# Optimization experiments

Measured on AMD Instinct MI355X. Metric: run time of the kernel, lower is better.

The kernel has to match this reference:

```python
import jax, jax.numpy as jnp
import numpy as np

N, C, OUT, S, NS = 8192, 256, 256, 8, 16  # points, in_planes, out_planes, share_planes, nsample
MID = OUT  # mid_planes = out_planes // 1
H = OUT // S  # linear_w bottleneck width
EPS = 1e-5


def _bn(x, g, b, m, v):
    # inference-mode BatchNorm1d over last (channel) dim
    return (x - m) * jax.lax.rsqrt(v + EPS) * g + b


def _knn_idx(p, k):
    # squared euclidean distances, (N,N); indices of k nearest (self included)
    sq = jnp.sum(p * p, axis=1)
    d = sq[:, None] + sq[None, :] - 2.0 * (p @ p.T)
    return jax.lax.top_k(-jax.lax.stop_gradient(d), k)[1]  # (N, k) int32


def setup_inputs() -> dict:
    key = jax.random.key(0)
    ks = jax.random.split(key, 24)
    g = lambda i, shape, s=0.05: jax.random.normal(ks[i], shape, jnp.float32) * s
    u = lambda i, shape: jax.random.uniform(ks[i], shape, dtype=jnp.float32)
    return {
        'p': u(0, (N, 3)),
        'x': g(1, (N, C), 1.0),
        'w_q': g(2, (C, MID)), 'b_q': jnp.zeros((MID,), jnp.float32),
        'w_k': g(3, (C, MID)), 'b_k': jnp.zeros((MID,), jnp.float32),
        'w_v': g(4, (C, OUT)), 'b_v': jnp.zeros((OUT,), jnp.float32),
        'p_w1': g(5, (3, 3), 0.5), 'p_b1': jnp.zeros((3,), jnp.float32),
        'p_bn_g': u(6, (3,)) + 0.5, 'p_bn_b': g(7, (3,), 0.1),
        'p_bn_m': g(8, (3,), 0.1), 'p_bn_v': u(9, (3,)) + 0.5,
        'p_w2': g(10, (3, OUT), 0.5), 'p_b2': jnp.zeros((OUT,), jnp.float32),
        'w_bn1_g': u(11, (MID,)) + 0.5, 'w_bn1_b': g(12, (MID,), 0.1),
        'w_bn1_m': g(13, (MID,), 0.1), 'w_bn1_v': u(14, (MID,)) + 0.5,
        'w_l1_w': g(15, (MID, H)), 'w_l1_b': jnp.zeros((H,), jnp.float32),
        'w_bn2_g': u(16, (H,)) + 0.5, 'w_bn2_b': g(17, (H,), 0.1),
        'w_bn2_m': g(18, (H,), 0.1), 'w_bn2_v': u(19, (H,)) + 0.5,
        'w_l2_w': g(20, (H, H)), 'w_l2_b': jnp.zeros((H,), jnp.float32),
    }


def reference(p, x, w_q, b_q, w_k, b_k, w_v, b_v,
              p_w1, p_b1, p_bn_g, p_bn_b, p_bn_m, p_bn_v, p_w2, p_b2,
              w_bn1_g, w_bn1_b, w_bn1_m, w_bn1_v, w_l1_w, w_l1_b,
              w_bn2_g, w_bn2_b, w_bn2_m, w_bn2_v, w_l2_w, w_l2_b):
    # PointTransformerLayer forward (single point cloud, o = [N])
    xq = x @ w_q + b_q            # (N, MID)
    xk = x @ w_k + b_k            # (N, MID)
    xv = x @ w_v + b_v            # (N, OUT)

    idx = _knn_idx(p, NS)         # (N, NS) KNN neighbor indices
    pr_xyz = p[idx] - p[:, None, :]   # (N, NS, 3) relative coords (with_xyz=True)
    xk_g = xk[idx]                # (N, NS, MID) gathered keys
    xv_g = xv[idx]                # (N, NS, OUT) gathered values

    # linear_p: Linear(3,3) -> BN -> ReLU -> Linear(3, OUT)
    pr = jax.nn.relu(_bn(pr_xyz @ p_w1 + p_b1, p_bn_g, p_bn_b, p_bn_m, p_bn_v))
    pr = pr @ p_w2 + p_b2         # (N, NS, OUT)

    # einops reduce 'n ns (i j)->n ns j' with j=MID is identity since MID==OUT
    r_qk = xk_g - xq[:, None, :] + pr   # (N, NS, MID)

    # linear_w: BN -> ReLU -> Linear(MID,H) -> BN -> ReLU -> Linear(H,H)
    w = jax.nn.relu(_bn(r_qk, w_bn1_g, w_bn1_b, w_bn1_m, w_bn1_v)) @ w_l1_w + w_l1_b
    w = jax.nn.relu(_bn(w, w_bn2_g, w_bn2_b, w_bn2_m, w_bn2_v)) @ w_l2_w + w_l2_b
    w = jax.nn.softmax(w, axis=1)       # softmax over neighbors (dim=1)

    v = (xv_g + pr).reshape(N, NS, S, H)      # 'n ns (s i) -> n ns s i'
    out = jnp.einsum('ntsi,nti->nsi', v, w)   # weighted aggregation over neighbors
    return out.reshape(N, OUT)
```

## Files before the change

### kernel.cpp

```cpp
#include <hip/hip_runtime.h>
#include <hip/hip_bf16.h>
#include <math.h>

#define N_PTS 8192
#define C_IN  256
#define OUT_C 256
#define NSAMP 16
#define H_W   32
#define EPSBN 1e-5f
#define GDIM  8
#define NCELL (GDIM * GDIM * GDIM)
#define CAPC  768
#define CAP_H 64

typedef short bf16x8 __attribute__((ext_vector_type(8)));
typedef float f32x4  __attribute__((ext_vector_type(4)));

__device__ __forceinline__ float dist2(const float4 a, const float4 b) {
  float dot = a.x * b.x + a.y * b.y + a.z * b.z;
  return a.w + b.w - 2.0f * dot;
}

__device__ __forceinline__ unsigned long long make_key(float d, int j) {
  unsigned int di = __float_as_uint(d);
  unsigned int ord = ((int)di >= 0) ? (di ^ 0x80000000u) : ~di;
  return ((unsigned long long)ord << 32) | (unsigned int)j;
}

__device__ __forceinline__ void chain_insert(unsigned long long (&ak)[16], unsigned long long key) {
  if (key < ak[0]) {
    #pragma unroll
    for (int s = 0; s < 15; ++s) {
      unsigned long long mn = ak[s] < key ? ak[s] : key;
      unsigned long long nx = ak[s + 1];
      ak[s] = nx > mn ? nx : mn;
    }
    ak[15] = ak[15] < key ? ak[15] : key;
  }
}

__device__ __forceinline__ float b2f(short s) {
  return __uint_as_float(((unsigned int)(unsigned short)s) << 16);
}
__device__ __forceinline__ short f2b(float v) {
  __hip_bfloat16 h = __float2bfloat16(v);
  short s;
  __builtin_memcpy(&s, &h, 2);
  return s;
}

__global__ __launch_bounds__(256) void prep_kernel(
    const float* __restrict__ p,
    const float* __restrict__ wq, const float* __restrict__ wk, const float* __restrict__ wv,
    const float* __restrict__ bq, const float* __restrict__ bk, const float* __restrict__ bv,
    const float* __restrict__ l1w, const float* __restrict__ l2w,
    const float* __restrict__ bn1g, const float* __restrict__ bn1b,
    const float* __restrict__ bn1m, const float* __restrict__ bn1v,
    float4* __restrict__ p4, __hip_bfloat16* __restrict__ Bp, float* __restrict__ biasp,
    __hip_bfloat16* __restrict__ l1wp, __hip_bfloat16* __restrict__ l2wp,
    float* __restrict__ sc1, float* __restrict__ of1,
    int* __restrict__ cursor, int* __restrict__ pt_cell) {
  int tid = blockIdx.x * blockDim.x + threadIdx.x;
  if (tid < 48 * 32 * 16 * 8) {
    int kj = tid & 7, n = (tid >> 3) & 15, kb = (tid >> 7) & 31, nt = tid >> 12;
    int k = kb * 8 + kj, col = nt * 16 + n;
    float v;
    if (col < 256)      v = wq[k * 256 + col];
    else if (col < 512) v = wk[k * 256 + (col - 256)];
    else                v = wv[k * 256 + (col - 512)];
    Bp[tid] = __float2bfloat16(v);
  }
  if (tid < 768) {
    biasp[tid] = tid < 256 ? bq[tid] : (tid < 512 ? bk[tid - 256] : bv[tid - 512]);
  }
  if (tid < 8192) {
    int kj = tid & 7, n = (tid >> 3) & 15, kb = (tid >> 7) & 31, nt = (tid >> 12) & 1;
    int k = kb * 8 + kj, col = nt * 16 + n;
    l1wp[tid] = __float2bfloat16(l1w[k * 32 + col]);
  }
  if (tid < 1024) {
    int kj = tid & 7, n = (tid >> 3) & 15, kb = (tid >> 7) & 3, nt = (tid >> 9) & 1;
    int k = kb * 8 + kj, col = nt * 16 + n;
    l2wp[tid] = __float2bfloat16(l2w[k * 32 + col]);
  }
  if (tid < 256) {
    float s1 = bn1g[tid] * rsqrtf(bn1v[tid] + EPSBN);
    sc1[tid] = s1;
    of1[tid] = bn1b[tid] - bn1m[tid] * s1;
  }
  if (tid < NCELL) cursor[tid] = 0;
  if (tid < N_PTS) {
    float px = p[tid * 3 + 0], py = p[tid * 3 + 1], pz = p[tid * 3 + 2];
    float sq = px * px;
    sq += py * py;
    sq += pz * pz;
    p4[tid] = make_float4(px, py, pz, sq);
    int cx = min(GDIM - 1, max(0, (int)(px * GDIM)));
    int cy = min(GDIM - 1, max(0, (int)(py * GDIM)));
    int cz = min(GDIM - 1, max(0, (int)(pz * GDIM)));
    pt_cell[tid] = (cz * GDIM + cy) * GDIM + cx;
  }
}

__global__ __launch_bounds__(512) void scatter_scan(
    const float4* __restrict__ p4, const int* __restrict__ pt_cell,
    int* __restrict__ cell_start, int* __restrict__ cursor,
    float4* __restrict__ sp4, int* __restrict__ sidx, int* __restrict__ rank) {
  __shared__ int buf[NCELL];
  const int t = threadIdx.x;
  buf[t] = 0;
  __syncthreads();
  for (int i = t; i < N_PTS; i += 512) atomicAdd(&buf[pt_cell[i]], 1);
  __syncthreads();
  for (int off = 1; off < NCELL; off <<= 1) {
    int add = (t >= off) ? buf[t - off] : 0;
    __syncthreads();
    buf[t] += add;
    __syncthreads();
  }
  if (blockIdx.x == 0) {
    cell_start[t + 1] = buf[t];
    if (t == 0) cell_start[0] = 0;
  }
  const int pid = blockIdx.x * 512 + t;
  const int c = pt_cell[pid];
  const int start = (c == 0) ? 0 : buf[c - 1];
  const int pos = start + atomicAdd(&cursor[c], 1);
  sp4[pos] = p4[pid];
  sidx[pos] = pid;
  rank[pid] = pos;
}

__global__ __launch_bounds__(256) void gemm_qkv_mfma(
    const float* __restrict__ x, const int* __restrict__ sidx,
    const __hip_bfloat16* __restrict__ Bp,
    const float* __restrict__ biasp, __hip_bfloat16* __restrict__ xqkv) {
  const int w = threadIdx.x >> 6;
  const int lane = threadIdx.x & 63;
  const int gw = blockIdx.x * 4 + w;
  const int m0 = (gw & 127) * 64;
  const int nt4 = (gw >> 7) * 4;
  const int n = lane & 15, q = lane >> 4;

  int o[4];
  #pragma unroll
  for (int mi = 0; mi < 4; ++mi) o[mi] = sidx[m0 + mi * 16 + n];

  f32x4 acc[4][4];
  #pragma unroll
  for (int mi = 0; mi < 4; ++mi)
    #pragma unroll
    for (int ni = 0; ni < 4; ++ni) acc[mi][ni] = (f32x4){0.f, 0.f, 0.f, 0.f};

  for (int k0 = 0; k0 < 256; k0 += 32) {
    bf16x8 af[4], bfr[4];
    #pragma unroll
    for (int mi = 0; mi < 4; ++mi) {
      const float* xr = &x[(size_t)o[mi] * 256 + k0 + q * 8];
      float4 xa = *(const float4*)xr;
      float4 xb = *(const float4*)(xr + 4);
      af[mi][0] = f2b(xa.x); af[mi][1] = f2b(xa.y);
      af[mi][2] = f2b(xa.z); af[mi][3] = f2b(xa.w);
      af[mi][4] = f2b(xb.x); af[mi][5] = f2b(xb.y);
      af[mi][6] = f2b(xb.z); af[mi][7] = f2b(xb.w);
    }
    #pragma unroll
    for (int ni = 0; ni < 4; ++ni)
      bfr[ni] = *(const bf16x8*)&Bp[(size_t)(nt4 + ni) * 4096 + (k0 >> 3) * 128 + q * 128 + n * 8];
    #pragma unroll
    for (int mi = 0; mi < 4; ++mi)
      #pragma unroll
      for (int ni = 0; ni < 4; ++ni)
        acc[mi][ni] = __builtin_amdgcn_mfma_f32_16x16x32_bf16(af[mi], bfr[ni], acc[mi][ni], 0, 0, 0);
  }
  #pragma unroll
  for (int ni = 0; ni < 4; ++ni) {
    int col = (nt4 + ni) * 16 + n;
    float b = biasp[col];
    #pragma unroll
    for (int mi = 0; mi < 4; ++mi)
      #pragma unroll
      for (int r = 0; r < 4; ++r)
        xqkv[(size_t)(m0 + mi * 16 + q * 4 + r) * 768 + col] = __float2bfloat16(acc[mi][ni][r] + b);
  }
}

__global__ __launch_bounds__(256) void knn_grid(
    const float4* __restrict__ sp4, const int* __restrict__ sidx,
    const int* __restrict__ cell_start, int* __restrict__ nbr) {
  __shared__ float4 cpos[CAPC];
  __shared__ int    cidx[CAPC];
  __shared__ unsigned long long hk_s[8][CAP_H];
  __shared__ unsigned long long okey_s[8][16];
  __shared__ float tv_s[8][64];
  __shared__ int cnt_s[8];
  __shared__ int cell_s0_s[27];
  __shared__ int len_s[27];
  __shared__ int pref_s[28];
  __shared__ int nc_s, total_s;

  const int cell = blockIdx.x >> 1;
  const int sub  = blockIdx.x & 1;
  const int tid = threadIdx.x;
  const int hcx = cell & 7, hcy = (cell >> 3) & 7, hcz = cell >> 6;
  const int cs = cell_start[cell], ce = cell_start[cell + 1];

  const int ax0 = max(hcx - 1, 0), ax1 = min(hcx + 1, GDIM - 1);
  const int ay0 = max(hcy - 1, 0), ay1 = min(hcy + 1, GDIM - 1);
  const int az0 = max(hcz - 1, 0), az1 = min(hcz + 1, GDIM - 1);
  const int nx = ax1 - ax0 + 1, ny = ay1 - ay0 + 1, nz = az1 - az0 + 1;
  const int nbc = nx * ny * nz;

  if (tid < nbc) {
    int cx = ax0 + tid % nx;
    int cy = ay0 + (tid / nx) % ny;
    int cz = az0 + tid / (nx * ny);
    int cc = (cz * GDIM + cy) * GDIM + cx;
    int s0 = cell_start[cc];
    cell_s0_s[tid] = s0;
    len_s[tid] = cell_start[cc + 1] - s0;
  }
  __syncthreads();
  if (tid == 0) {
    int off = 0;
    for (int m = 0; m < nbc; ++m) { pref_s[m] = off; off += len_s[m]; }
    pref_s[nbc] = off;
    nc_s = nbc;
    total_s = off;
  }
  __syncthreads();
  const int nc = nc_s, total = total_s;

  for (int idx = tid; idx < total && idx < CAPC; idx += 256) {
    int c = 0;
    while (c + 1 < nc && pref_s[c + 1] <= idx) ++c;
    int g = cell_s0_s[c] + (idx - pref_s[c]);
    cpos[idx] = sp4[g];
    cidx[idx] = sidx[g];
  }
  __syncthreads();

  const int ptl = tid >> 5, slice = tid & 31;

  for (int p0 = cs + 8 * sub; p0 < ce; p0 += 16) {
    const int np = min(8, ce - p0);
    const bool pok = ptl < np;
    const int ld = pok ? (p0 + ptl) : cs;
    const float4 pi = sp4[ld];
    const int orig = sidx[ld];

    if (tid < 8) cnt_s[tid] = 0;
    if (tid < 128) okey_s[tid >> 4][tid & 15] = ~0ULL;
    __syncthreads();

    float t0 = 3.0e38f, t1 = 3.0e38f;
    for (int idx = slice; idx < total; idx += 32) {
      float4 q;
      if (idx < CAPC) q = cpos[idx];
      else {
        int c = 0;
        while (c + 1 < nc && pref_s[c + 1] <= idx) ++c;
        q = sp4[cell_s0_s[c] + (idx - pref_s[c])];
      }
      float d = dist2(pi, q);
      if (d < t1) {
        if (d < t0) { t1 = t0; t0 = d; } else { t1 = d; }
      }
    }
    tv_s[ptl][slice * 2]     = t0;
    tv_s[ptl][slice * 2 + 1] = t1;
    __syncthreads();

    int r0 = 0, r1 = 0;
    #pragma unroll 8
    for (int j = 0; j < 64; ++j) {
      float wv = tv_s[ptl][j];
      r0 += (wv < t0) ? 1 : 0;
      r1 += (wv < t1) ? 1 : 0;
    }
    float cand = fmaxf(r0 <= 15 ? t0 : -3.0e38f, r1 <= 15 ? t1 : -3.0e38f);
    cand = fmaxf(cand, __shfl_xor(cand, 1, 64));
    cand = fmaxf(cand, __shfl_xor(cand, 2, 64));
    cand = fmaxf(cand, __shfl_xor(cand, 4, 64));
    cand = fmaxf(cand, __shfl_xor(cand, 8, 64));
    cand = fmaxf(cand, __shfl_xor(cand, 16, 64));
    const float d16 = cand;

    if (pok) {
      for (int idx = slice; idx < total; idx += 32) {
        float4 q;
        int qi;
        if (idx < CAPC) { q = cpos[idx]; qi = cidx[idx]; }
        else {
          int c = 0;
          while (c + 1 < nc && pref_s[c + 1] <= idx) ++c;
          int g = cell_s0_s[c] + (idx - pref_s[c]);
          q = sp4[g]; qi = sidx[g];
        }
        float d = dist2(pi, q);
        if (d <= d16) {
          int pos = atomicAdd(&cnt_s[ptl], 1);
          if (pos < CAP_H) hk_s[ptl][pos] = make_key(d, qi);
        }
      }
    }
    __syncthreads();

    const int cntr = cnt_s[ptl];
    const bool overflow = cntr > CAP_H;
    const int cnt = overflow ? 0 : cntr;

    if (pok) {
      for (int i = slice; i < cnt; i += 32) {
        unsigned long long key = hk_s[ptl][i];
        int rk = 0;
        for (int j = 0; j < cnt; ++j) rk += (hk_s[ptl][j] < key) ? 1 : 0;
        if (rk < 16) okey_s[ptl][rk] = key;
      }
    }
    __syncthreads();

    if (slice == 0 && pok) {
      unsigned long long akm[16];
      if (!overflow) {
        #pragma unroll
        for (int s = 0; s < 16; ++s) akm[s] = okey_s[ptl][15 - s];
      } else {
        #pragma unroll
        for (int s = 0; s < 16; ++s) akm[s] = ~0ULL;
        for (int idx = 0; idx < total; ++idx) {
          float4 q; int qi;
          if (idx < CAPC) { q = cpos[idx]; qi = cidx[idx]; }
          else {
            int c = 0;
            while (c + 1 < nc && pref_s[c + 1] <= idx) ++c;
            int g = cell_s0_s[c] + (idx - pref_s[c]);
            q = sp4[g]; qi = sidx[g];
          }
          chain_insert(akm, make_key(dist2(pi, q), qi));
        }
      }
      float r;
      if (akm[0] == ~0ULL) {
        r = 1e9f;
      } else {
        unsigned int ord = (unsigned int)(akm[0] >> 32);
        unsigned int di = (ord & 0x80000000u) ? (ord ^ 0x80000000u) : ~ord;
        float dd = __uint_as_float(di);
        r = sqrtf(fmaxf(dd, 0.f)) * 1.001f + 1e-4f;
      }
      int lx = (int)fminf(fmaxf(floorf((pi.x - r) * GDIM), 0.f), (float)(GDIM - 1));
      int ux = (int)fminf(fmaxf(floorf((pi.x + r) * GDIM), 0.f), (float)(GDIM - 1));
      int ly = (int)fminf(fmaxf(floorf((pi.y - r) * GDIM), 0.f), (float)(GDIM - 1));
      int uy = (int)fminf(fmaxf(floorf((pi.y + r) * GDIM), 0.f), (float)(GDIM - 1));
      int lz = (int)fminf(fmaxf(floorf((pi.z - r) * GDIM), 0.f), (float)(GDIM - 1));
      int uz = (int)fminf(fmaxf(floorf((pi.z + r) * GDIM), 0.f), (float)(GDIM - 1));
      if (lx < ax0 || ux > ax1 || ly < ay0 || uy > ay1 || lz < az0 || uz > az1) {
        for (int cz = lz; cz <= uz; ++cz)
          for (int cy = ly; cy <= uy; ++cy)
            for (int cx = lx; cx <= ux; ++cx) {
              if (cx >= ax0 && cx <= ax1 && cy >= ay0 && cy <= ay1 && cz >= az0 && cz <= az1)
                continue;
              int cc = (cz * GDIM + cy) * GDIM + cx;
              int s0 = cell_start[cc], e0 = cell_start[cc + 1];
              for (int k = s0; k < e0; ++k) {
                float4 q = sp4[k];
                chain_insert(akm, make_key(dist2(pi, q), sidx[k]));
              }
            }
      }
      #pragma unroll
      for (int s = 0; s < 16; ++s) nbr[orig * NSAMP + s] = (int)(akm[s] & 0xFFFFFFFFu);
    }
    __syncthreads();
  }
}

__global__ __launch_bounds__(256) void fused_pt(
    const float4* __restrict__ sp4, const int* __restrict__ sidx, const int* __restrict__ rank,
    const __hip_bfloat16* __restrict__ xqkv, const int* __restrict__ nbr,
    const float* __restrict__ pw1, const float* __restrict__ pb1,
    const float* __restrict__ pbng, const float* __restrict__ pbnb,
    const float* __restrict__ pbnm, const float* __restrict__ pbnv,
    const float* __restrict__ pw2, const float* __restrict__ pb2,
    const float* __restrict__ sc1, const float* __restrict__ of1,
    const __hip_bfloat16* __restrict__ l1wp, const float* __restrict__ l1b,
    const float* __restrict__ bn2g, const float* __restrict__ bn2b,
    const float* __restrict__ bn2m, const float* __restrict__ bn2v,
    const __hip_bfloat16* __restrict__ l2wp, const float* __restrict__ l2b,
    float* __restrict__ out) {
  __shared__ __align__(16) __hip_bfloat16 a_s[2][NSAMP][264];
  __shared__ __align__(16) __hip_bfloat16 h1_s[2][NSAMP][40];
  __shared__ float w_s[2][NSAMP][33];
  __shared__ float q3_s[2][NSAMP][4];
  __shared__ int jn[2][NSAMP];
  __shared__ float psum[2][2][264];
  __shared__ int iorig[2];

  const int b0 = blockIdx.x * 2;
  const int tid = threadIdx.x;

  if (tid < 32) {
    int spt = tid >> 4, t = tid & 15;
    int b = b0 + spt;
    int i = sidx[b];
    if (t == 0) iorig[spt] = i;
    int j = nbr[i * NSAMP + t];
    int k = rank[j];
    jn[spt][t] = k;
    float4 pj = sp4[k];
    float4 pc = sp4[b];
    float rx = pj.x - pc.x;
    float ry = pj.y - pc.y;
    float rz = pj.z - pc.z;
    #pragma unroll
    for (int c3 = 0; c3 < 3; ++c3) {
      float t2 = rx * pw1[0 * 3 + c3] + ry * pw1[1 * 3 + c3] + rz * pw1[2 * 3 + c3] + pb1[c3];
      t2 = (t2 - pbnm[c3]) * rsqrtf(pbnv[c3] + EPSBN) * pbng[c3] + pbnb[c3];
      q3_s[spt][t][c3] = fmaxf(t2, 0.f);
    }
  }
  __syncthreads();

  const int pt = tid >> 7;
  const int t127 = tid & 127;
  const int g = t127 >> 5;
  const int cg = (t127 & 31) * 8;
  const int b = b0 + pt;

  float xqv[8], s1v[8], o1v[8], w20v[8], w21v[8], w22v[8], pb2v[8];
  {
    bf16x8 xq8 = *(const bf16x8*)&xqkv[(size_t)b * 768 + cg];
    #pragma unroll
    for (int u = 0; u < 8; ++u) {
      int c = cg + u;
      xqv[u] = b2f(xq8[u]);
      s1v[u] = sc1[c];
      o1v[u] = of1[c];
      w20v[u] = pw2[c];
      w21v[u] = pw2[256 + c];
      w22v[u] = pw2[512 + c];
      pb2v[u] = pb2[c];
    }
  }

  #pragma unroll
  for (int pass = 0; pass < 4; ++pass) {
    int t = g + pass * 4;
    int k = jn[pt][t];
    float q30 = q3_s[pt][t][0], q31 = q3_s[pt][t][1], q32 = q3_s[pt][t][2];
    bf16x8 xk8 = *(const bf16x8*)&xqkv[(size_t)k * 768 + 256 + cg];
    bf16x8 av;
    #pragma unroll
    for (int u = 0; u < 8; ++u) {
      float prv = q30 * w20v[u] + q31 * w21v[u] + q32 * w22v[u] + pb2v[u];
      float r = b2f(xk8[u]) - xqv[u] + prv;
      av[u] = f2b(fmaxf(r * s1v[u] + o1v[u], 0.f));
    }
    *(bf16x8*)&a_s[pt][t][cg] = av;
  }
  __syncthreads();

  const int w = tid >> 6;
  const int lane = tid & 63;
  const int mpt = w >> 1, hh = w & 1;
  const int nn = lane & 15, q = lane >> 4;
  {
    f32x4 acc = {0.f, 0.f, 0.f, 0.f};
    #pragma unroll
    for (int k0 = 0; k0 < 256; k0 += 32) {
      bf16x8 a = *(const bf16x8*)&a_s[mpt][nn][k0 + q * 8];
      bf16x8 bb = *(const bf16x8*)&l1wp[hh * 4096 + (k0 >> 3) * 128 + q * 128 + nn * 8];
      acc = __builtin_amdgcn_mfma_f32_16x16x32_bf16(a, bb, acc, 0, 0, 0);
    }
    int h = hh * 16 + nn;
    float s2 = bn2g[h] * rsqrtf(bn2v[h] + EPSBN);
    float o2 = bn2b[h] - bn2m[h] * s2;
    float l1bh = l1b[h];
    #pragma unroll
    for (int r = 0; r < 4; ++r)
      h1_s[mpt][q * 4 + r][h] = __float2bfloat16(fmaxf((acc[r] + l1bh) * s2 + o2, 0.f));
  }
  __syncthreads();

  {
    bf16x8 a = *(const bf16x8*)&h1_s[mpt][nn][q * 8];
    bf16x8 bb = *(const bf16x8*)&l2wp[hh * 512 + q * 128 + nn * 8];
    f32x4 z = {0.f, 0.f, 0.f, 0.f};
    f32x4 d = __builtin_amdgcn_mfma_f32_16x16x32_bf16(a, bb, z, 0, 0, 0);
    int h = hh * 16 + nn;
    float l2bh = l2b[h];
    #pragma unroll
    for (int r = 0; r < 4; ++r) w_s[mpt][q * 4 + r][h] = d[r] + l2bh;
  }
  __syncthreads();

  if (tid < 64) {
    int spt = tid >> 5, h = tid & 31;
    float m = -1e30f;
    #pragma unroll
    for (int t = 0; t < NSAMP; ++t) m = fmaxf(m, w_s[spt][t][h]);
    float e[NSAMP];
    float ssum = 0.f;
    #pragma unroll
    for (int t = 0; t < NSAMP; ++t) { e[t] = __expf(w_s[spt][t][h] - m); ssum += e[t]; }
    float inv = 1.f / ssum;
    #pragma unroll
    for (int t = 0; t < NSAMP; ++t) w_s[spt][t][h] = e[t] * inv;
  }
  __syncthreads();

  const int hb = cg & 31;
  float acc8[8];
  #pragma unroll
  for (int u = 0; u < 8; ++u) acc8[u] = 0.f;
  #pragma unroll
  for (int pass = 0; pass < 4; ++pass) {
    int t = g + pass * 4;
    int k = jn[pt][t];
    float q30 = q3_s[pt][t][0], q31 = q3_s[pt][t][1], q32 = q3_s[pt][t][2];
    bf16x8 xv8 = *(const bf16x8*)&xqkv[(size_t)k * 768 + 512 + cg];
    #pragma unroll
    for (int u = 0; u < 8; ++u) {
      float prv = q30 * w20v[u] + q31 * w21v[u] + q32 * w22v[u] + pb2v[u];
      acc8[u] += (b2f(xv8[u]) + prv) * w_s[pt][t][hb + u];
    }
  }
  #pragma unroll
  for (int u = 0; u < 8; ++u) acc8[u] += __shfl_xor(acc8[u], 32, 64);
  if ((lane >> 5) == 0) {
    #pragma unroll
    for (int u = 0; u < 8; ++u) psum[mpt][hh][cg + u] = acc8[u];
  }
  __syncthreads();
  {
    int opt = tid >> 7;
    int c0 = (tid & 127) * 2;
    float v0 = psum[opt][0][c0] + psum[opt][1][c0];
    float v1 = psum[opt][0][c0 + 1] + psum[opt][1][c0 + 1];
    int io = iorig[opt];
    *(float2*)&out[(size_t)io * OUT_C + c0] = make_float2(v0, v1);
  }
}

extern "C" void kernel_launch(void* const* d_in, const int* in_sizes, int n_in,
                              void* d_out, int out_size, void* d_ws, size_t ws_size,
                              hipStream_t stream) {
  const float* p    = (const float*)d_in[0];
  const float* x    = (const float*)d_in[1];
  const float* wq   = (const float*)d_in[2];
  const float* bq   = (const float*)d_in[3];
  const float* wk   = (const float*)d_in[4];
  const float* bk   = (const float*)d_in[5];
  const float* wv   = (const float*)d_in[6];
  const float* bv   = (const float*)d_in[7];
  const float* pw1  = (const float*)d_in[8];
  const float* pb1  = (const float*)d_in[9];
  const float* pbng = (const float*)d_in[10];
  const float* pbnb = (const float*)d_in[11];
  const float* pbnm = (const float*)d_in[12];
  const float* pbnv = (const float*)d_in[13];
  const float* pw2  = (const float*)d_in[14];
  const float* pb2  = (const float*)d_in[15];
  const float* bn1g = (const float*)d_in[16];
  const float* bn1b = (const float*)d_in[17];
  const float* bn1m = (const float*)d_in[18];
  const float* bn1v = (const float*)d_in[19];
  const float* l1w  = (const float*)d_in[20];
  const float* l1b  = (const float*)d_in[21];
  const float* bn2g = (const float*)d_in[22];
  const float* bn2b = (const float*)d_in[23];
  const float* bn2m = (const float*)d_in[24];
  const float* bn2v = (const float*)d_in[25];
  const float* l2w  = (const float*)d_in[26];
  const float* l2b  = (const float*)d_in[27];
  float* out = (float*)d_out;

  char* ws = (char*)d_ws;
  float4* p4       = (float4*)(ws + 0x000000);
  float*  biasp    = (float*)(ws + 0x040000);
  int*    cursor   = (int*)(ws + 0x042800);
  int*    cell_st  = (int*)(ws + 0x043000);
  int*    pt_cell  = (int*)(ws + 0x044000);
  float4* sp4      = (float4*)(ws + 0x050000);
  int*    sidx     = (int*)(ws + 0x070000);
  __hip_bfloat16* l1wp = (__hip_bfloat16*)(ws + 0x080000);
  __hip_bfloat16* l2wp = (__hip_bfloat16*)(ws + 0x084000);
  float*  sc1      = (float*)(ws + 0x085000);
  float*  of1      = (float*)(ws + 0x085800);
  int*    rank     = (int*)(ws + 0x088000);
  int*    nbr      = (int*)(ws + 0x090000);
  __hip_bfloat16* Bp   = (__hip_bfloat16*)(ws + 0x110000);
  __hip_bfloat16* xqkv = (__hip_bfloat16*)(ws + 0x570000);

  prep_kernel<<<dim3(768), dim3(256), 0, stream>>>(
      p, wq, wk, wv, bq, bk, bv, l1w, l2w, bn1g, bn1b, bn1m, bn1v,
      p4, Bp, biasp, l1wp, l2wp, sc1, of1, cursor, pt_cell);
  scatter_scan<<<dim3(16), dim3(512), 0, stream>>>(
      p4, pt_cell, cell_st, cursor, sp4, sidx, rank);
  knn_grid<<<dim3(NCELL * 2), dim3(256), 0, stream>>>(sp4, sidx, cell_st, nbr);
  gemm_qkv_mfma<<<dim3(384), dim3(256), 0, stream>>>(x, sidx, Bp, biasp, xqkv);
  fused_pt<<<dim3(N_PTS / 2), dim3(256), 0, stream>>>(
      sp4, sidx, rank, xqkv, nbr, pw1, pb1, pbng, pbnb, pbnm, pbnv, pw2, pb2,
      sc1, of1, l1wp, l1b, bn2g, bn2b, bn2m, bn2v, l2wp, l2b, out);
}
```

Before: 201.8 us.

## Merge KNN and QKV GEMM into one launch and pre-convert x to bf16

After: 198.3 us. Within noise of the previous version (-1.7%).

```diff
diff --git a/kernel.cpp b/kernel.cpp
--- a/kernel.cpp
+++ b/kernel.cpp
@@ -50,17 +50,27 @@
 }
 
 __global__ __launch_bounds__(256) void prep_kernel(
-    const float* __restrict__ p,
+    const float* __restrict__ p, const float* __restrict__ x,
     const float* __restrict__ wq, const float* __restrict__ wk, const float* __restrict__ wv,
     const float* __restrict__ bq, const float* __restrict__ bk, const float* __restrict__ bv,
     const float* __restrict__ l1w, const float* __restrict__ l2w,
     const float* __restrict__ bn1g, const float* __restrict__ bn1b,
     const float* __restrict__ bn1m, const float* __restrict__ bn1v,
     float4* __restrict__ p4, __hip_bfloat16* __restrict__ Bp, float* __restrict__ biasp,
+    __hip_bfloat16* __restrict__ xb,
     __hip_bfloat16* __restrict__ l1wp, __hip_bfloat16* __restrict__ l2wp,
     float* __restrict__ sc1, float* __restrict__ of1,
     int* __restrict__ cursor, int* __restrict__ pt_cell) {
   int tid = blockIdx.x * blockDim.x + threadIdx.x;
+  if (tid < 262144) {
+    const float* xr = &x[(size_t)tid * 8];
+    float4 xa = *(const float4*)xr;
+    float4 xc = *(const float4*)(xr + 4);
+    bf16x8 v;
+    v[0] = f2b(xa.x); v[1] = f2b(xa.y); v[2] = f2b(xa.z); v[3] = f2b(xa.w);
+    v[4] = f2b(xc.x); v[5] = f2b(xc.y); v[6] = f2b(xc.z); v[7] = f2b(xc.w);
+    *(bf16x8*)&xb[(size_t)tid * 8] = v;
+  }
   if (tid < 48 * 32 * 16 * 8) {
     int kj = tid & 7, n = (tid >> 3) & 15, kb = (tid >> 7) & 31, nt = tid >> 12;
     int k = kb * 8 + kj, col = nt * 16 + n;
@@ -131,63 +141,56 @@
   rank[pid] = pos;
 }
 
-__global__ __launch_bounds__(256) void gemm_qkv_mfma(
-    const float* __restrict__ x, const int* __restrict__ sidx,
-    const __hip_bfloat16* __restrict__ Bp,
+__global__ __launch_bounds__(256) void knn_gemm(
+    const float4* __restrict__ sp4, const int* __restrict__ sidx,
+    const int* __restrict__ cell_start, int* __restrict__ nbr,
+    const __hip_bfloat16* __restrict__ xb, const __hip_bfloat16* __restrict__ Bp,
     const float* __restrict__ biasp, __hip_bfloat16* __restrict__ xqkv) {
-  const int w = threadIdx.x >> 6;
-  const int lane = threadIdx.x & 63;
-  const int gw = blockIdx.x * 4 + w;
-  const int m0 = (gw & 127) * 64;
-  const int nt4 = (gw >> 7) * 4;
-  const int n = lane & 15, q = lane >> 4;
-
-  int o[4];
-  #pragma unroll
-  for (int mi = 0; mi < 4; ++mi) o[mi] = sidx[m0 + mi * 16 + n];
-
-  f32x4 acc[4][4];
-  #pragma unroll
-  for (int mi = 0; mi < 4; ++mi)
-    #pragma unroll
-    for (int ni = 0; ni < 4; ++ni) acc[mi][ni] = (f32x4){0.f, 0.f, 0.f, 0.f};
-
-  for (int k0 = 0; k0 < 256; k0 += 32) {
-    bf16x8 af[4], bfr[4];
-    #pragma unroll
-    for (int mi = 0; mi < 4; ++mi) {
-      const float* xr = &x[(size_t)o[mi] * 256 + k0 + q * 8];
-      float4 xa = *(const float4*)xr;
-      float4 xb = *(const float4*)(xr + 4);
-      af[mi][0] = f2b(xa.x); af[mi][1] = f2b(xa.y);
-      af[mi][2] = f2b(xa.z); af[mi][3] = f2b(xa.w);
-      af[mi][4] = f2b(xb.x); af[mi][5] = f2b(xb.y);
-      af[mi][6] = f2b(xb.z); af[mi][7] = f2b(xb.w);
-    }
-    #pragma unroll
-    for (int ni = 0; ni < 4; ++ni)
-      bfr[ni] = *(const bf16x8*)&Bp[(size_t)(nt4 + ni) * 4096 + (k0 >> 3) * 128 + q * 128 + n * 8];
+  if (blockIdx.x >= NCELL * 2) {
+    const int w = threadIdx.x >> 6;
+    const int lane = threadIdx.x & 63;
+    const int gw = (blockIdx.x - NCELL * 2) * 4 + w;
+    const int m0 = (gw & 127) * 64;
+    const int nt4 = (gw >> 7) * 4;
+    const int n = lane & 15, q = lane >> 4;
+
+    int o[4];
+    #pragma unroll
+    for (int mi = 0; mi < 4; ++mi) o[mi] = sidx[m0 + mi * 16 + n];
+
+    f32x4 acc[4][4];
     #pragma unroll
     for (int mi = 0; mi < 4; ++mi)
       #pragma unroll
+      for (int ni = 0; ni < 4; ++ni) acc[mi][ni] = (f32x4){0.f, 0.f, 0.f, 0.f};
+
+    for (int k0 = 0; k0 < 256; k0 += 32) {
+      bf16x8 af[4], bfr[4];
+      #pragma unroll
+      for (int mi = 0; mi < 4; ++mi)
+        af[mi] = *(const bf16x8*)&xb[(size_t)o[mi] * 256 + k0 + q * 8];
+      #pragma unroll
       for (int ni = 0; ni < 4; ++ni)
-        acc[mi][ni] = __builtin_amdgcn_mfma_f32_16x16x32_bf16(af[mi], bfr[ni], acc[mi][ni], 0, 0, 0);
-  }
-  #pragma unroll
-  for (int ni = 0; ni < 4; ++ni) {
-    int col = (nt4 + ni) * 16 + n;
-    float b = biasp[col];
-    #pragma unroll
-    for (int mi = 0; mi < 4; ++mi)
+        bfr[ni] = *(const bf16x8*)&Bp[(size_t)(nt4 + ni) * 4096 + (k0 >> 3) * 128 + q * 128 + n * 8];
       #pragma unroll
-      for (int r = 0; r < 4; ++r)
-        xqkv[(size_t)(m0 + mi * 16 + q * 4 + r) * 768 + col] = __float2bfloat16(acc[mi][ni][r] + b);
-  }
-}
-
-__global__ __launch_bounds__(256) void knn_grid(
-    const float4* __restrict__ sp4, const int* __restrict__ sidx,
-    const int* __restrict__ cell_start, int* __restrict__ nbr) {
+      for (int mi = 0; mi < 4; ++mi)
+        #pragma unroll
+        for (int ni = 0; ni < 4; ++ni)
+          acc[mi][ni] = __builtin_amdgcn_mfma_f32_16x16x32_bf16(af[mi], bfr[ni], acc[mi][ni], 0, 0, 0);
+    }
+    #pragma unroll
+    for (int ni = 0; ni < 4; ++ni) {
+      int col = (nt4 + ni) * 16 + n;
+      float b = biasp[col];
+      #pragma unroll
+      for (int mi = 0; mi < 4; ++mi)
+        #pragma unroll
+        for (int r = 0; r < 4; ++r)
+          xqkv[(size_t)(m0 + mi * 16 + q * 4 + r) * 768 + col] = __float2bfloat16(acc[mi][ni][r] + b);
+    }
+    return;
+  }
+
   __shared__ float4 cpos[CAPC];
   __shared__ int    cidx[CAPC];
   __shared__ unsigned long long hk_s[8][CAP_H];
@@ -591,15 +594,16 @@
   int*    rank     = (int*)(ws + 0x088000);
   int*    nbr      = (int*)(ws + 0x090000);
   __hip_bfloat16* Bp   = (__hip_bfloat16*)(ws + 0x110000);
+  __hip_bfloat16* xb   = (__hip_bfloat16*)(ws + 0x170000);
   __hip_bfloat16* xqkv = (__hip_bfloat16*)(ws + 0x570000);
 
-  prep_kernel<<<dim3(768), dim3(256), 0, stream>>>(
-      p, wq, wk, wv, bq, bk, bv, l1w, l2w, bn1g, bn1b, bn1m, bn1v,
-      p4, Bp, biasp, l1wp, l2wp, sc1, of1, cursor, pt_cell);
+  prep_kernel<<<dim3(1024), dim3(256), 0, stream>>>(
+      p, x, wq, wk, wv, bq, bk, bv, l1w, l2w, bn1g, bn1b, bn1m, bn1v,
+      p4, Bp, biasp, xb, l1wp, l2wp, sc1, of1, cursor, pt_cell);
   scatter_scan<<<dim3(16), dim3(512), 0, stream>>>(
       p4, pt_cell, cell_st, cursor, sp4, sidx, rank);
-  knn_grid<<<dim3(NCELL * 2), dim3(256), 0, stream>>>(sp4, sidx, cell_st, nbr);
-  gemm_qkv_mfma<<<dim3(384), dim3(256), 0, stream>>>(x, sidx, Bp, biasp, xqkv);
+  knn_gemm<<<dim3(NCELL * 2 + 384), dim3(256), 0, stream>>>(
+      sp4, sidx, cell_st, nbr, xb, Bp, biasp, xqkv);
   fused_pt<<<dim3(N_PTS / 2), dim3(256), 0, stream>>>(
       sp4, sidx, rank, xqkv, nbr, pw1, pb1, pbng, pbnb, pbnm, pbnv, pw2, pb2,
       sc1, of1, l1wp, l1b, bn2g, bn2b, bn2m, bn2v, l2wp, l2b, out);
```
